# Optimization experiments

Measured on AMD Instinct MI355X. Metric: run time of the kernel, lower is better.

The kernel has to match this reference:

```python
import jax, jax.numpy as jnp
import numpy as np

N, D_MODEL, D_FFN, K = 8192, 1024, 4096, 512


def setup_inputs() -> dict:
    key = jax.random.key(0)
    ks = jax.random.split(key, 5)
    x = jax.random.normal(ks[0], (N, D_MODEL), dtype=jnp.float32)
    topk_indices = jax.random.randint(ks[1], (N, K), 0, D_FFN, dtype=jnp.int32)
    scale = 0.02
    w_gate = jax.random.normal(ks[2], (D_MODEL, D_FFN), dtype=jnp.float32) * scale
    w_up = jax.random.normal(ks[3], (D_MODEL, D_FFN), dtype=jnp.float32) * scale
    w_down = jax.random.normal(ks[4], (D_FFN, D_MODEL), dtype=jnp.float32) * scale
    return {"x": x, "topk_indices": topk_indices, "w_gate": w_gate, "w_up": w_up, "w_down": w_down}


def reference(x, topk_indices, w_gate, w_up, w_down):
    # Dense gate/up projections: [N, d_ffn]
    G = x @ w_gate
    U = x @ w_up
    # Gather only the top-k active neurons per token and fuse SwiGLU there.
    G_act = jnp.take_along_axis(G, topk_indices, axis=1)  # [N, k]
    U_act = jnp.take_along_axis(U, topk_indices, axis=1)  # [N, k]
    Z_active = jax.nn.silu(G_act) * U_act                 # [N, k]
    # Sparse-to-dense down projection: scatter active activations back into
    # the d_ffn axis (zeros elsewhere), then dense matmul with w_down.
    n, k = topk_indices.shape
    rows = jnp.arange(n, dtype=topk_indices.dtype)[:, None]
    Z_dense = jnp.zeros((n, w_down.shape[0]), dtype=Z_active.dtype).at[rows, topk_indices].add(Z_active)
    return Z_dense @ w_down  # [N, d_model]
```

## Files before the change

### kernel.cpp

```cpp
#include <hip/hip_runtime.h>
#include <hip/hip_bf16.h>
#include <cstdint>
#include <cstddef>

#define N_TOK   8192
#define D_MODEL 1024
#define D_FFN   4096
#define K_TOP   512
#define NHALF   2048

typedef __bf16 bf16_t;
typedef __bf16 bf16x8 __attribute__((ext_vector_type(8)));
typedef __bf16 bf16x4 __attribute__((ext_vector_type(4)));
typedef float  f32x4  __attribute__((ext_vector_type(4)));


__global__ void cvt_f32_bf16(const float* __restrict__ in, bf16_t* __restrict__ out, int n4) {
  int i = blockIdx.x * blockDim.x + threadIdx.x;
  if (i < n4) {
    const f32x4 v = ((const f32x4*)in)[i];
    bf16x4 o;
    o[0] = (bf16_t)v[0]; o[1] = (bf16_t)v[1]; o[2] = (bf16_t)v[2]; o[3] = (bf16_t)v[3];
    ((bf16x4*)out)[i] = o;
  }
}

__global__ void transpose_cvt(const float* __restrict__ in, bf16_t* __restrict__ out,
                              int rows, int cols) {
  __shared__ float tile[32][33];
  const int tx = threadIdx.x, ty = threadIdx.y;
  const int x = blockIdx.x * 32 + tx;
#pragma unroll
  for (int i = 0; i < 32; i += 8) {
    int y = blockIdx.y * 32 + ty + i;
    tile[ty + i][tx] = in[(size_t)y * cols + x];
  }
  __syncthreads();
  const int xo = blockIdx.y * 32 + tx;
#pragma unroll
  for (int i = 0; i < 32; i += 8) {
    int yo = blockIdx.x * 32 + ty + i;
    out[(size_t)yo * rows + xo] = (bf16_t)tile[tx][ty + i];
  }
}

#define ROWS_PER_BLK 4
__global__ __launch_bounds__(256) void count_scatter_lds(
    const int* __restrict__ idx, unsigned int* __restrict__ M) {
  __shared__ unsigned int loc[ROWS_PER_BLK * (D_FFN / 8)];
  const int t = threadIdx.x;
  const int r0 = blockIdx.x * ROWS_PER_BLK;

#pragma unroll
  for (int i = 0; i < ROWS_PER_BLK * (D_FFN / 8) / 256; ++i)
    loc[t + i * 256] = 0;
  __syncthreads();

  const int* ip = idx + (size_t)r0 * K_TOP;
#pragma unroll
  for (int i = 0; i < ROWS_PER_BLK * K_TOP / 256; ++i) {
    const int e = t + i * 256;
    const int lr = e >> 9;
    const int j = ip[e];
    atomicAdd(&loc[lr * (D_FFN / 8) + (j >> 3)], 1u << ((j & 7) * 4));
  }
  __syncthreads();

  unsigned int* op = M + (size_t)r0 * (D_FFN / 8);
#pragma unroll
  for (int i = 0; i < ROWS_PER_BLK * (D_FFN / 8) / 256; ++i)
    op[t + i * 256] = loc[t + i * 256];
}


__device__ __forceinline__ void gload_lds16(const void* g, void* l) {
#if __has_builtin(__builtin_amdgcn_global_load_lds)
  __builtin_amdgcn_global_load_lds((__attribute__((address_space(1))) void*)(g),
                                   (__attribute__((address_space(3))) void*)(l), 16, 0, 0);
#else
  *(bf16x8*)l = *(const bf16x8*)g;
#endif
}

#define BM1 256
#define BN1 128
#define BK1 64
#define NT1 (D_MODEL / BK1)
#define LDSBUF 65536

__global__ __launch_bounds__(512, 2) void gemm_gateup_8p(
    const bf16_t* __restrict__ A,
    const bf16_t* __restrict__ Bg,
    const bf16_t* __restrict__ Bu,
    const unsigned int* __restrict__ cnt,
    bf16_t* __restrict__ Z,
    int n_base)
{
  extern __shared__ char smem[];
  const int t = threadIdx.x;
  const int lane = t & 63;
  const int w = t >> 6;
  const int wr = w >> 1;
  const int wc = w & 1;
  const int l15 = lane & 15;
  const int grp = lane >> 4;
  const int m0 = blockIdx.x * BM1;
  const int n0 = blockIdx.y * BN1;

  int offA[4], offB[2];
#pragma unroll
  for (int c = 0; c < 4; ++c) {
    const int s = c * 512 + w * 64 + lane;
    const int r = s >> 3, cb = (s & 7) ^ (r & 7);
    offA[c] = (m0 + r) * D_MODEL + cb * 8;
  }
#pragma unroll
  for (int c = 0; c < 2; ++c) {
    const int s = c * 512 + w * 64 + lane;
    const int r = s >> 3, cb = (s & 7) ^ (r & 7);
    offB[c] = (n_base + n0 + r) * D_MODEL + cb * 8;
  }
  const int dst0 = (w * 64 + lane) * 16;

  const int swz = l15 & 7;
  const int a_k0 = wr * 8192 + l15 * 128 + ((0 + grp) ^ swz) * 16;
  const int a_k1 = wr * 8192 + l15 * 128 + ((4 + grp) ^ swz) * 16;
  const int bg_k0 = 32768 + wc * 8192 + l15 * 128 + ((0 + grp) ^ swz) * 16;
  const int bg_k1 = 32768 + wc * 8192 + l15 * 128 + ((4 + grp) ^ swz) * 16;
  const int bu_k0 = bg_k0 + 16384;
  const int bu_k1 = bg_k1 + 16384;

#pragma unroll
  for (int c = 0; c < 4; ++c) gload_lds16(A + offA[c], smem + dst0 + c * 8192);
#pragma unroll
  for (int c = 0; c < 2; ++c) gload_lds16(Bg + offB[c], smem + 32768 + dst0 + c * 8192);
#pragma unroll
  for (int c = 0; c < 2; ++c) gload_lds16(Bu + offB[c], smem + 49152 + dst0 + c * 8192);
  asm volatile("s_waitcnt vmcnt(0)" ::: "memory");
  __builtin_amdgcn_s_barrier();

  f32x4 accg[4][4] = {};
  f32x4 accu[4][4] = {};

#define MFMA16(ACC, AF, BF)                                                      \
  _Pragma("unroll")                                                              \
  for (int m = 0; m < 4; ++m)                                                    \
    _Pragma("unroll")                                                            \
    for (int n = 0; n < 4; ++n)                                                  \
      ACC[m][n] = __builtin_amdgcn_mfma_f32_16x16x32_bf16(AF[m], BF[n], ACC[m][n], 0, 0, 0);

#define PHASE_SYNC_PRE()                                                         \
  __builtin_amdgcn_s_barrier();                                                  \
  asm volatile("s_waitcnt lgkmcnt(0)" ::: "memory");                             \
  __builtin_amdgcn_sched_barrier(0);                                             \
  __builtin_amdgcn_s_setprio(1);

#define PHASE_SYNC_POST()                                                        \
  __builtin_amdgcn_s_setprio(0);                                                 \
  __builtin_amdgcn_s_barrier();

  for (int tt = 0; tt < NT1; ++tt) {
    char* rb = smem + (tt & 1) * LDSBUF;
    char* wb = smem + ((tt & 1) ^ 1) * LDSBUF;
    const int kg = (tt + 1) * BK1;
    const bool st = (tt + 1 < NT1);
    bf16x8 af[4], bgf[4], buf_[4];

#pragma unroll
    for (int m = 0; m < 4; ++m) af[m] = *(const bf16x8*)(rb + a_k0 + m * 2048);
#pragma unroll
    for (int n = 0; n < 4; ++n) bgf[n] = *(const bf16x8*)(rb + bg_k0 + n * 2048);
    if (st) {
      gload_lds16(A + offA[0] + kg, wb + dst0);
      gload_lds16(A + offA[1] + kg, wb + dst0 + 8192);
    }
    PHASE_SYNC_PRE();
    MFMA16(accg, af, bgf);
    PHASE_SYNC_POST();

#pragma unroll
    for (int n = 0; n < 4; ++n) buf_[n] = *(const bf16x8*)(rb + bu_k0 + n * 2048);
    if (st) {
      gload_lds16(A + offA[2] + kg, wb + dst0 + 16384);
      gload_lds16(A + offA[3] + kg, wb + dst0 + 24576);
    }
    PHASE_SYNC_PRE();
    MFMA16(accu, af, buf_);
    PHASE_SYNC_POST();

#pragma unroll
    for (int m = 0; m < 4; ++m) af[m] = *(const bf16x8*)(rb + a_k1 + m * 2048);
#pragma unroll
    for (int n = 0; n < 4; ++n) bgf[n] = *(const bf16x8*)(rb + bg_k1 + n * 2048);
    if (st) {
      gload_lds16(Bg + offB[0] + kg, wb + 32768 + dst0);
      gload_lds16(Bg + offB[1] + kg, wb + 32768 + dst0 + 8192);
    }
    PHASE_SYNC_PRE();
    MFMA16(accg, af, bgf);
    PHASE_SYNC_POST();

#pragma unroll
    for (int n = 0; n < 4; ++n) buf_[n] = *(const bf16x8*)(rb + bu_k1 + n * 2048);
    if (st) {
      gload_lds16(Bu + offB[0] + kg, wb + 49152 + dst0);
      gload_lds16(Bu + offB[1] + kg, wb + 49152 + dst0 + 8192);
    }
    __builtin_amdgcn_s_barrier();
    asm volatile("s_waitcnt lgkmcnt(0)" ::: "memory");
    __builtin_amdgcn_sched_barrier(0);
    __builtin_amdgcn_s_setprio(1);
    MFMA16(accu, af, buf_);
    __builtin_amdgcn_s_setprio(0);
    if (st) asm volatile("s_waitcnt vmcnt(0)" ::: "memory");
    __builtin_amdgcn_s_barrier();
  }

#pragma unroll
  for (int m = 0; m < 4; ++m) {
#pragma unroll
    for (int n = 0; n < 4; ++n) {
      const int colL = n0 + wc * 64 + n * 16 + l15;
      const int jg = n_base + colL;
#pragma unroll
      for (int j = 0; j < 4; ++j) {
        const int row = m0 + wr * 64 + m * 16 + grp * 4 + j;
        float g = accg[m][n][j];
        float u = accu[m][n][j];
        unsigned int cw = cnt[(size_t)row * (D_FFN / 8) + (jg >> 3)];
        float c = (float)((cw >> ((jg & 7) * 4)) & 15u);
        float z = c * u * (g / (1.0f + __expf(-g)));
        Z[(size_t)row * NHALF + colL] = (bf16_t)z;
      }
    }
  }
#undef MFMA16
#undef PHASE_SYNC_PRE
#undef PHASE_SYNC_POST
}

#define BK 32
#define BM2 64
#define BN2 128

__global__ __launch_bounds__(256, 4) void gemm_down(
    const bf16_t* __restrict__ A,
    const bf16_t* __restrict__ B,
    float* __restrict__ C,
    int k_base, int accum)
{
  __shared__ alignas(16) bf16_t As[BM2 * BK];
  __shared__ alignas(16) bf16_t Bs[BN2 * BK];

  const int m0 = blockIdx.x * BM2;
  const int n0 = blockIdx.y * BN2;
  const int t = threadIdx.x;
  const int lane = t & 63;
  const int w = t >> 6;
  const int wr = w >> 1, wc = w & 1;
  const int l15 = lane & 15;
  const int kk = (lane >> 4) * 8;

  const int rowi = t >> 2;
  const int coli = (t & 3) * 8;
  const bf16_t* pA = A + (size_t)(m0 + rowi) * NHALF + coli;
  const bf16_t* pB = B + (size_t)(n0 + rowi) * D_FFN + k_base + coli;
  const size_t rstepB = (size_t)64 * D_FFN;

  f32x4 acc[2][4] = {};

  for (int k0 = 0; k0 < NHALF; k0 += BK) {
    gload_lds16(pA,          As + t * 8);
    gload_lds16(pB,          Bs + t * 8);
    gload_lds16(pB + rstepB, Bs + (256 + t) * 8);
    pA += BK; pB += BK;
    __syncthreads();

    bf16x8 af[2], bf[4];
#pragma unroll
    for (int m = 0; m < 2; ++m)
      af[m] = *(const bf16x8*)(As + (wr * 32 + m * 16 + l15) * BK + kk);
#pragma unroll
    for (int n = 0; n < 4; ++n)
      bf[n] = *(const bf16x8*)(Bs + (wc * 64 + n * 16 + l15) * BK + kk);
#pragma unroll
    for (int m = 0; m < 2; ++m)
#pragma unroll
      for (int n = 0; n < 4; ++n)
        acc[m][n] = __builtin_amdgcn_mfma_f32_16x16x32_bf16(af[m], bf[n], acc[m][n], 0, 0, 0);
    __syncthreads();
  }

#pragma unroll
  for (int m = 0; m < 2; ++m) {
#pragma unroll
    for (int n = 0; n < 4; ++n) {
      const int col = n0 + wc * 64 + n * 16 + l15;
#pragma unroll
      for (int j = 0; j < 4; ++j) {
        const int row = m0 + wr * 32 + m * 16 + (lane >> 4) * 4 + j;
        const size_t off = (size_t)row * D_MODEL + col;
        float prev = accum ? C[off] : 0.0f;
        C[off] = prev + acc[m][n][j];
      }
    }
  }
}


extern "C" void kernel_launch(void* const* d_in, const int* in_sizes, int n_in,
                              void* d_out, int out_size, void* d_ws, size_t ws_size,
                              hipStream_t stream) {
  const float* x  = (const float*)d_in[0];
  const int*   idx = (const int*)d_in[1];
  const float* wg = (const float*)d_in[2];
  const float* wu = (const float*)d_in[3];
  const float* wd = (const float*)d_in[4];
  float* out = (float*)d_out;

  char* ws = (char*)d_ws;
  const size_t SZ_XB  = (size_t)N_TOK * D_MODEL * 2;
  const size_t SZ_W   = (size_t)D_MODEL * D_FFN * 2;
  const size_t SZ_CNT = (size_t)N_TOK * D_FFN / 2;
  bf16_t* xb  = (bf16_t*)(ws);
  bf16_t* wgT = (bf16_t*)(ws + SZ_XB);
  bf16_t* wuT = (bf16_t*)(ws + SZ_XB + SZ_W);
  bf16_t* wdT = (bf16_t*)(ws + SZ_XB + 2 * SZ_W);
  unsigned int* cnt = (unsigned int*)(ws + SZ_XB + 3 * SZ_W);
  bf16_t* Z   = (bf16_t*)(ws + SZ_XB + 3 * SZ_W + SZ_CNT);

  (void)hipFuncSetAttribute((const void*)gemm_gateup_8p,
                            hipFuncAttributeMaxDynamicSharedMemorySize, 131072);

  count_scatter_lds<<<N_TOK / ROWS_PER_BLK, 256, 0, stream>>>(idx, cnt);
  cvt_f32_bf16<<<(N_TOK * D_MODEL / 4 + 255) / 256, 256, 0, stream>>>(x, xb, N_TOK * D_MODEL / 4);
  transpose_cvt<<<dim3(D_FFN / 32, D_MODEL / 32), dim3(32, 8), 0, stream>>>(wg, wgT, D_MODEL, D_FFN);
  transpose_cvt<<<dim3(D_FFN / 32, D_MODEL / 32), dim3(32, 8), 0, stream>>>(wu, wuT, D_MODEL, D_FFN);
  transpose_cvt<<<dim3(D_MODEL / 32, D_FFN / 32), dim3(32, 8), 0, stream>>>(wd, wdT, D_FFN, D_MODEL);

  gemm_gateup_8p<<<dim3(N_TOK / BM1, NHALF / BN1), 512, 131072, stream>>>(xb, wgT, wuT, cnt, Z, 0);
  gemm_down<<<dim3(N_TOK / BM2, D_MODEL / BN2), 256, 0, stream>>>(Z, wdT, out, 0, 0);
  gemm_gateup_8p<<<dim3(N_TOK / BM1, NHALF / BN1), 512, 131072, stream>>>(xb, wgT, wuT, cnt, Z, NHALF);
  gemm_down<<<dim3(N_TOK / BM2, D_MODEL / BN2), 256, 0, stream>>>(Z, wdT, out, NHALF, 1);
}
```

Measured before the change: 298.0 us.

## Replace down-projection GEMM with 256x128 double-buffered swizzled LDS kernel

Replaces the small 64x128, BK=32 down-projection GEMM with a 512-thread, 256x128 tile kernel. It uses BK=64, double-buffered swizzled LDS, direct global-to-LDS loads and the same phase/priority scheduling as the gate/up kernel. This is meant to raise data reuse per tile and overlap loads with MFMA work. Separately, the gate/up kernel now issues all next-tile prefetch loads at the first phase instead of spreading them across four phases. The larger tiles cut the down-GEMM grid to 256 blocks, which may leave some CUs underused, and 96KB of LDS limits occupancy.

```diff
diff --git a/kernel.cpp b/kernel.cpp
--- a/kernel.cpp
+++ b/kernel.cpp
@@ -81,6 +81,23 @@
   *(bf16x8*)l = *(const bf16x8*)g;
 #endif
 }
+
+#define MFMA16(ACC, AF, BF)                                                      \
+  _Pragma("unroll")                                                              \
+  for (int m = 0; m < 4; ++m)                                                    \
+    _Pragma("unroll")                                                            \
+    for (int n = 0; n < 4; ++n)                                                  \
+      ACC[m][n] = __builtin_amdgcn_mfma_f32_16x16x32_bf16(AF[m], BF[n], ACC[m][n], 0, 0, 0);
+
+#define PHASE_SYNC_PRE()                                                         \
+  __builtin_amdgcn_s_barrier();                                                  \
+  asm volatile("s_waitcnt lgkmcnt(0)" ::: "memory");                             \
+  __builtin_amdgcn_sched_barrier(0);                                             \
+  __builtin_amdgcn_s_setprio(1);
+
+#define PHASE_SYNC_POST()                                                        \
+  __builtin_amdgcn_s_setprio(0);                                                 \
+  __builtin_amdgcn_s_barrier();
 
 #define BM1 256
 #define BN1 128
@@ -142,23 +159,6 @@
   f32x4 accg[4][4] = {};
   f32x4 accu[4][4] = {};
 
-#define MFMA16(ACC, AF, BF)                                                      \
-  _Pragma("unroll")                                                              \
-  for (int m = 0; m < 4; ++m)                                                    \
-    _Pragma("unroll")                                                            \
-    for (int n = 0; n < 4; ++n)                                                  \
-      ACC[m][n] = __builtin_amdgcn_mfma_f32_16x16x32_bf16(AF[m], BF[n], ACC[m][n], 0, 0, 0);
-
-#define PHASE_SYNC_PRE()                                                         \
-  __builtin_amdgcn_s_barrier();                                                  \
-  asm volatile("s_waitcnt lgkmcnt(0)" ::: "memory");                             \
-  __builtin_amdgcn_sched_barrier(0);                                             \
-  __builtin_amdgcn_s_setprio(1);
-
-#define PHASE_SYNC_POST()                                                        \
-  __builtin_amdgcn_s_setprio(0);                                                 \
-  __builtin_amdgcn_s_barrier();
-
   for (int tt = 0; tt < NT1; ++tt) {
     char* rb = smem + (tt & 1) * LDSBUF;
     char* wb = smem + ((tt & 1) ^ 1) * LDSBUF;
@@ -171,8 +171,12 @@
 #pragma unroll
     for (int n = 0; n < 4; ++n) bgf[n] = *(const bf16x8*)(rb + bg_k0 + n * 2048);
     if (st) {
-      gload_lds16(A + offA[0] + kg, wb + dst0);
-      gload_lds16(A + offA[1] + kg, wb + dst0 + 8192);
+#pragma unroll
+      for (int c = 0; c < 4; ++c) gload_lds16(A + offA[c] + kg, wb + dst0 + c * 8192);
+#pragma unroll
+      for (int c = 0; c < 2; ++c) gload_lds16(Bg + offB[c] + kg, wb + 32768 + dst0 + c * 8192);
+#pragma unroll
+      for (int c = 0; c < 2; ++c) gload_lds16(Bu + offB[c] + kg, wb + 49152 + dst0 + c * 8192);
     }
     PHASE_SYNC_PRE();
     MFMA16(accg, af, bgf);
@@ -180,10 +184,6 @@
 
 #pragma unroll
     for (int n = 0; n < 4; ++n) buf_[n] = *(const bf16x8*)(rb + bu_k0 + n * 2048);
-    if (st) {
-      gload_lds16(A + offA[2] + kg, wb + dst0 + 16384);
-      gload_lds16(A + offA[3] + kg, wb + dst0 + 24576);
-    }
     PHASE_SYNC_PRE();
     MFMA16(accu, af, buf_);
     PHASE_SYNC_POST();
@@ -192,20 +192,12 @@
     for (int m = 0; m < 4; ++m) af[m] = *(const bf16x8*)(rb + a_k1 + m * 2048);
 #pragma unroll
     for (int n = 0; n < 4; ++n) bgf[n] = *(const bf16x8*)(rb + bg_k1 + n * 2048);
-    if (st) {
-      gload_lds16(Bg + offB[0] + kg, wb + 32768 + dst0);
-      gload_lds16(Bg + offB[1] + kg, wb + 32768 + dst0 + 8192);
-    }
     PHASE_SYNC_PRE();
     MFMA16(accg, af, bgf);
     PHASE_SYNC_POST();
 
 #pragma unroll
     for (int n = 0; n < 4; ++n) buf_[n] = *(const bf16x8*)(rb + bu_k1 + n * 2048);
-    if (st) {
-      gload_lds16(Bu + offB[0] + kg, wb + 49152 + dst0);
-      gload_lds16(Bu + offB[1] + kg, wb + 49152 + dst0 + 8192);
-    }
     __builtin_amdgcn_s_barrier();
     asm volatile("s_waitcnt lgkmcnt(0)" ::: "memory");
     __builtin_amdgcn_sched_barrier(0);
@@ -234,71 +226,104 @@
       }
     }
   }
-#undef MFMA16
-#undef PHASE_SYNC_PRE
-#undef PHASE_SYNC_POST
-}
-
-#define BK 32
-#define BM2 64
+}
+
+#define BM2 256
 #define BN2 128
-
-__global__ __launch_bounds__(256, 4) void gemm_down(
+#define BK2 64
+#define NT2 (NHALF / BK2)
+#define LDSBUF2 49152
+
+__global__ __launch_bounds__(512, 2) void gemm_down_8p(
     const bf16_t* __restrict__ A,
     const bf16_t* __restrict__ B,
     float* __restrict__ C,
     int k_base, int accum)
 {
-  __shared__ alignas(16) bf16_t As[BM2 * BK];
-  __shared__ alignas(16) bf16_t Bs[BN2 * BK];
-
-  const int m0 = blockIdx.x * BM2;
-  const int n0 = blockIdx.y * BN2;
+  extern __shared__ char smem[];
   const int t = threadIdx.x;
   const int lane = t & 63;
   const int w = t >> 6;
-  const int wr = w >> 1, wc = w & 1;
+  const int wr = w >> 1;
+  const int wc = w & 1;
   const int l15 = lane & 15;
-  const int kk = (lane >> 4) * 8;
-
-  const int rowi = t >> 2;
-  const int coli = (t & 3) * 8;
-  const bf16_t* pA = A + (size_t)(m0 + rowi) * NHALF + coli;
-  const bf16_t* pB = B + (size_t)(n0 + rowi) * D_FFN + k_base + coli;
-  const size_t rstepB = (size_t)64 * D_FFN;
-
-  f32x4 acc[2][4] = {};
-
-  for (int k0 = 0; k0 < NHALF; k0 += BK) {
-    gload_lds16(pA,          As + t * 8);
-    gload_lds16(pB,          Bs + t * 8);
-    gload_lds16(pB + rstepB, Bs + (256 + t) * 8);
-    pA += BK; pB += BK;
-    __syncthreads();
-
-    bf16x8 af[2], bf[4];
-#pragma unroll
-    for (int m = 0; m < 2; ++m)
-      af[m] = *(const bf16x8*)(As + (wr * 32 + m * 16 + l15) * BK + kk);
-#pragma unroll
-    for (int n = 0; n < 4; ++n)
-      bf[n] = *(const bf16x8*)(Bs + (wc * 64 + n * 16 + l15) * BK + kk);
-#pragma unroll
-    for (int m = 0; m < 2; ++m)
-#pragma unroll
-      for (int n = 0; n < 4; ++n)
-        acc[m][n] = __builtin_amdgcn_mfma_f32_16x16x32_bf16(af[m], bf[n], acc[m][n], 0, 0, 0);
-    __syncthreads();
-  }
-
-#pragma unroll
-  for (int m = 0; m < 2; ++m) {
+  const int grp = lane >> 4;
+  const int m0 = blockIdx.x * BM2;
+  const int n0 = blockIdx.y * BN2;
+
+  int offA[4], offB[2];
+#pragma unroll
+  for (int c = 0; c < 4; ++c) {
+    const int s = c * 512 + w * 64 + lane;
+    const int r = s >> 3, cb = (s & 7) ^ (r & 7);
+    offA[c] = (m0 + r) * NHALF + cb * 8;
+  }
+#pragma unroll
+  for (int c = 0; c < 2; ++c) {
+    const int s = c * 512 + w * 64 + lane;
+    const int r = s >> 3, cb = (s & 7) ^ (r & 7);
+    offB[c] = (n0 + r) * D_FFN + k_base + cb * 8;
+  }
+  const int dst0 = (w * 64 + lane) * 16;
+
+  const int swz = l15 & 7;
+  const int a_k0 = wr * 8192 + l15 * 128 + ((0 + grp) ^ swz) * 16;
+  const int a_k1 = wr * 8192 + l15 * 128 + ((4 + grp) ^ swz) * 16;
+  const int b_k0 = 32768 + wc * 8192 + l15 * 128 + ((0 + grp) ^ swz) * 16;
+  const int b_k1 = 32768 + wc * 8192 + l15 * 128 + ((4 + grp) ^ swz) * 16;
+
+#pragma unroll
+  for (int c = 0; c < 4; ++c) gload_lds16(A + offA[c], smem + dst0 + c * 8192);
+#pragma unroll
+  for (int c = 0; c < 2; ++c) gload_lds16(B + offB[c], smem + 32768 + dst0 + c * 8192);
+  asm volatile("s_waitcnt vmcnt(0)" ::: "memory");
+  __builtin_amdgcn_s_barrier();
+
+  f32x4 acc[4][4] = {};
+
+  for (int tt = 0; tt < NT2; ++tt) {
+    char* rb = smem + (tt & 1) * LDSBUF2;
+    char* wb = smem + ((tt & 1) ^ 1) * LDSBUF2;
+    const int kg = (tt + 1) * BK2;
+    const bool st = (tt + 1 < NT2);
+    bf16x8 af[4], bf[4];
+
+#pragma unroll
+    for (int m = 0; m < 4; ++m) af[m] = *(const bf16x8*)(rb + a_k0 + m * 2048);
+#pragma unroll
+    for (int n = 0; n < 4; ++n) bf[n] = *(const bf16x8*)(rb + b_k0 + n * 2048);
+    if (st) {
+#pragma unroll
+      for (int c = 0; c < 4; ++c) gload_lds16(A + offA[c] + kg, wb + dst0 + c * 8192);
+#pragma unroll
+      for (int c = 0; c < 2; ++c) gload_lds16(B + offB[c] + kg, wb + 32768 + dst0 + c * 8192);
+    }
+    PHASE_SYNC_PRE();
+    MFMA16(acc, af, bf);
+    PHASE_SYNC_POST();
+
+#pragma unroll
+    for (int m = 0; m < 4; ++m) af[m] = *(const bf16x8*)(rb + a_k1 + m * 2048);
+#pragma unroll
+    for (int n = 0; n < 4; ++n) bf[n] = *(const bf16x8*)(rb + b_k1 + n * 2048);
+    __builtin_amdgcn_s_barrier();
+    asm volatile("s_waitcnt lgkmcnt(0)" ::: "memory");
+    __builtin_amdgcn_sched_barrier(0);
+    __builtin_amdgcn_s_setprio(1);
+    MFMA16(acc, af, bf);
+    __builtin_amdgcn_s_setprio(0);
+    if (st) asm volatile("s_waitcnt vmcnt(0)" ::: "memory");
+    __builtin_amdgcn_s_barrier();
+  }
+
+#pragma unroll
+  for (int m = 0; m < 4; ++m) {
 #pragma unroll
     for (int n = 0; n < 4; ++n) {
       const int col = n0 + wc * 64 + n * 16 + l15;
 #pragma unroll
       for (int j = 0; j < 4; ++j) {
-        const int row = m0 + wr * 32 + m * 16 + (lane >> 4) * 4 + j;
+        const int row = m0 + wr * 64 + m * 16 + grp * 4 + j;
         const size_t off = (size_t)row * D_MODEL + col;
         float prev = accum ? C[off] : 0.0f;
         C[off] = prev + acc[m][n][j];
@@ -331,6 +356,8 @@
 
   (void)hipFuncSetAttribute((const void*)gemm_gateup_8p,
                             hipFuncAttributeMaxDynamicSharedMemorySize, 131072);
+  (void)hipFuncSetAttribute((const void*)gemm_down_8p,
+                            hipFuncAttributeMaxDynamicSharedMemorySize, 98304);
 
   count_scatter_lds<<<N_TOK / ROWS_PER_BLK, 256, 0, stream>>>(idx, cnt);
   cvt_f32_bf16<<<(N_TOK * D_MODEL / 4 + 255) / 256, 256, 0, stream>>>(x, xb, N_TOK * D_MODEL / 4);
@@ -339,7 +366,7 @@
   transpose_cvt<<<dim3(D_MODEL / 32, D_FFN / 32), dim3(32, 8), 0, stream>>>(wd, wdT, D_FFN, D_MODEL);
 
   gemm_gateup_8p<<<dim3(N_TOK / BM1, NHALF / BN1), 512, 131072, stream>>>(xb, wgT, wuT, cnt, Z, 0);
-  gemm_down<<<dim3(N_TOK / BM2, D_MODEL / BN2), 256, 0, stream>>>(Z, wdT, out, 0, 0);
+  gemm_down_8p<<<dim3(N_TOK / BM2, D_MODEL / BN2), 512, 98304, stream>>>(Z, wdT, out, 0, 0);
   gemm_gateup_8p<<<dim3(N_TOK / BM1, NHALF / BN1), 512, 131072, stream>>>(xb, wgT, wuT, cnt, Z, NHALF);
-  gemm_down<<<dim3(N_TOK / BM2, D_MODEL / BN2), 256, 0, stream>>>(Z, wdT, out, NHALF, 1);
-}
+  gemm_down_8p<<<dim3(N_TOK / BM2, D_MODEL / BN2), 512, 98304, stream>>>(Z, wdT, out, NHALF, 1);
+}
```

After: 270.2 us. 9.3% less time.
